# Optimization experiments

Measured on AMD Instinct MI355X. Metric: run time of the kernel, lower is better.

Reference implementation:

```python
import jax, jax.numpy as jnp
import numpy as np

H, KV, D = 12, 2, 128        # q heads, kv heads, head_dim
HID = 1536
B, S = 4, 2048               # equal-length packed sequences
T = B * S
EPS = 1e-6
ROPE_THETA = 10000.0


def _rms_norm(x, w):
    # RMSNorm over last dim in fp32, as in Qwen3RMSNorm
    xf = x.astype(jnp.float32)
    var = jnp.mean(xf * xf, axis=-1, keepdims=True)
    return (w * (xf * jax.lax.rsqrt(var + EPS))).astype(x.dtype)


def _apply_rope(x, cos, sin):
    # x: [T, h, D]; cos/sin: [T, D/2] -> expand over heads
    half = cos.shape[-1]
    x1, x2 = x[..., :half], x[..., half:2 * half]
    c = cos[:, None, :]
    s = sin[:, None, :]
    return jnp.concatenate([x1 * c - x2 * s, x1 * s + x2 * c], axis=-1)


def setup_inputs() -> dict:
    key = jax.random.key(0)
    ks = jax.random.split(key, 8)
    hidden_states = jax.random.normal(ks[0], (T, HID), dtype=jnp.float32)
    # real RoPE tables over per-sequence positions
    inv_freq = 1.0 / (ROPE_THETA ** (np.arange(0, D, 2, dtype=np.float32) / D))  # [D/2]
    pos = np.tile(np.arange(S, dtype=np.float32), B)                              # [T]
    ang = pos[:, None] * inv_freq[None, :]
    cos = jnp.asarray(np.cos(ang), dtype=jnp.float32)
    sin = jnp.asarray(np.sin(ang), dtype=jnp.float32)
    sc = 0.02
    Wq = jax.random.normal(ks[1], (HID, H * D), dtype=jnp.float32) * sc
    Wk = jax.random.normal(ks[2], (HID, KV * D), dtype=jnp.float32) * sc
    Wv = jax.random.normal(ks[3], (HID, KV * D), dtype=jnp.float32) * sc
    Wo = jax.random.normal(ks[4], (H * D, HID), dtype=jnp.float32) * sc
    q_norm_w = jnp.ones((D,), dtype=jnp.float32)
    k_norm_w = jnp.ones((D,), dtype=jnp.float32)
    cu_seqlens = jnp.arange(B + 1, dtype=jnp.int32) * S
    return {"hidden_states": hidden_states, "cos": cos, "sin": sin,
            "Wq": Wq, "Wk": Wk, "Wv": Wv, "Wo": Wo,
            "q_norm_w": q_norm_w, "k_norm_w": k_norm_w,
            "cu_seqlens": cu_seqlens}


def reference(hidden_states, cos, sin, Wq, Wk, Wv, Wo, q_norm_w, k_norm_w, cu_seqlens):
    # QKV projections on packed tokens
    q = (hidden_states @ Wq).reshape(T, H, D)
    k = (hidden_states @ Wk).reshape(T, KV, D)
    v = (hidden_states @ Wv).reshape(T, KV, D)
    # Qwen3 per-head QK RMSNorm, then RoPE
    q = _apply_rope(_rms_norm(q, q_norm_w), cos, sin)
    k = _apply_rope(_rms_norm(k, k_norm_w), cos, sin)
    # equal-length sequences: unpack to [B, h, S, D] (block-diagonal varlen attn)
    qb = q.reshape(B, S, H, D).transpose(0, 2, 1, 3)
    kb = k.reshape(B, S, KV, D).transpose(0, 2, 1, 3)
    vb = v.reshape(B, S, KV, D).transpose(0, 2, 1, 3)
    # GQA: repeat kv heads
    rep = H // KV
    kb = jnp.repeat(kb, rep, axis=1)
    vb = jnp.repeat(vb, rep, axis=1)
    scale = D ** -0.5
    scores = jnp.einsum('bhqd,bhkd->bhqk', qb, kb) * scale
    causal = jnp.tril(jnp.ones((S, S), dtype=bool))
    scores = jnp.where(causal[None, None], scores, jnp.finfo(scores.dtype).min)
    attn = jax.nn.softmax(scores, axis=-1)
    out = jnp.einsum('bhqk,bhkd->bhqd', attn, vb)       # [B,H,S,D]
    out = out.transpose(0, 2, 1, 3).reshape(T, H * D)   # repack
    return out @ Wo
```

## Files before the change

kernel.cpp:

```cpp
#include <hip/hip_runtime.h>
#include <hip/hip_bf16.h>
#include <stdint.h>

#define H_   12
#define KV_  2
#define D_   128
#define HID_ 1536
#define B_   4
#define S_   2048
#define T_   (B_*S_)

typedef __attribute__((ext_vector_type(8))) short  bf16x8;
typedef __attribute__((ext_vector_type(4))) float  f32x4;

__device__ __forceinline__ ushort f2bf(float f) {
  union { float f; uint32_t u; } v; v.f = f;
  uint32_t u = v.u;
  return (ushort)((u + 0x7fffu + ((u >> 16) & 1u)) >> 16);
}
__device__ __forceinline__ float bf2f(ushort u) {
  union { uint32_t u; float f; } v; v.u = ((uint32_t)u) << 16;
  return v.f;
}
__device__ __forceinline__ uint32_t cvtpk_bf16(float lo, float hi) {
  uint32_t r;
  asm("v_cvt_pk_bf16_f32 %0, %1, %2" : "=v"(r) : "v"(lo), "v"(hi));
  return r;
}

__device__ __forceinline__ void gload_lds16(const void* g, void* l) {
  __builtin_amdgcn_global_load_lds(
      (const __attribute__((address_space(1))) uint32_t*)g,
      (__attribute__((address_space(3))) uint32_t*)l, 16, 0, 0);
}

__global__ __launch_bounds__(256) void transpose_cvt2(const float* __restrict__ W0,
                                                      ushort* __restrict__ Wt0,
                                                      const float* __restrict__ W1,
                                                      ushort* __restrict__ Wt1,
                                                      int K, int N) {
  __shared__ float tile[32][33];
  const float* W  = blockIdx.z ? W1  : W0;
  ushort*      Wt = blockIdx.z ? Wt1 : Wt0;
  int k0 = blockIdx.x * 32, n0 = blockIdx.y * 32;
  int tx = threadIdx.x & 31, ty = threadIdx.x >> 5;
#pragma unroll
  for (int i = 0; i < 32; i += 8)
    tile[ty + i][tx] = W[(long)(k0 + ty + i) * N + n0 + tx];
  __syncthreads();
#pragma unroll
  for (int i = 0; i < 32; i += 8)
    Wt[(long)(n0 + ty + i) * K + k0 + tx] = f2bf(tile[tx][ty + i]);
}

template <int OUT_F32>
__global__ __launch_bounds__(256, 2) void gemm_bt(const ushort* __restrict__ A,
                                                  const ushort* __restrict__ Bt,
                                                  void* __restrict__ Cv,
                                                  int M, int N, int K, int lda) {
  __shared__ ushort lA[128 * 32];
  __shared__ ushort lB[128 * 32];
  const int tid = threadIdx.x;
  const int lane = tid & 63, w = tid >> 6;
  const int wr = w >> 1, wc = w & 1;
  const int l15 = lane & 15, lh = lane >> 4;
  const long m0 = (long)blockIdx.x * 128, n0 = (long)blockIdx.y * 128;
  const ushort* Ab = A + m0 * lda;
  const ushort* Bb = Bt + n0 * K;
  const int sr = tid >> 2;
  const int sc = (tid & 3) * 8;
  const int ldsoff = w * 512;
  f32x4 acc[4][4] = {};

  for (int k0 = 0; k0 < K; k0 += 32) {
#pragma unroll
    for (int it = 0; it < 2; ++it) {
      gload_lds16(Ab + (long)(it * 64 + sr) * lda + k0 + sc, &lA[it * 2048 + ldsoff]);
      gload_lds16(Bb + (long)(it * 64 + sr) * K + k0 + sc, &lB[it * 2048 + ldsoff]);
    }
    __syncthreads();
    bf16x8 af[4], bfr[4];
    const int ra = (wr * 64 + l15) * 32 + lh * 8;
    const int rb = (wc * 64 + l15) * 32 + lh * 8;
#pragma unroll
    for (int i = 0; i < 4; ++i) {
      af[i]  = *(const bf16x8*)&lA[ra + i * 16 * 32];
      bfr[i] = *(const bf16x8*)&lB[rb + i * 16 * 32];
    }
#pragma unroll
    for (int i = 0; i < 4; ++i)
#pragma unroll
      for (int j = 0; j < 4; ++j)
        acc[i][j] = __builtin_amdgcn_mfma_f32_16x16x32_bf16(af[i], bfr[j], acc[i][j], 0, 0, 0);
    __syncthreads();
  }
#pragma unroll
  for (int i = 0; i < 4; ++i) {
#pragma unroll
    for (int q = 0; q < 4; ++q) {
      long row = m0 + wr * 64 + i * 16 + lh * 4 + q;
#pragma unroll
      for (int j = 0; j < 4; ++j) {
        long col = n0 + wc * 64 + j * 16 + l15;
        float v = acc[i][j][q];
        if (OUT_F32) ((float*)Cv)[row * N + col] = v;
        else         ((ushort*)Cv)[row * N + col] = f2bf(v);
      }
    }
  }
}

__global__ __launch_bounds__(512) void gemm256f(const float* __restrict__ A32,
                                                const ushort* __restrict__ Bt,
                                                ushort* __restrict__ Cv,
                                                int M, int N, int K, int lda) {
  __shared__ ushort lA[2][256 * 64];
  __shared__ ushort lB[2][256 * 64];
  const int tid = threadIdx.x, lane = tid & 63;
  const int w = tid >> 6;
  const int l15 = lane & 15, lh = lane >> 4;
  const int wr = w >> 2, wc = w & 3;
  const long m0 = (long)blockIdx.x * 256, n0 = (long)blockIdx.y * 256;
  const float*  Ab = A32 + m0 * lda;
  const ushort* Bb = Bt + n0 * K;
  const int swz = (l15 & 7) << 4;

  f32x4 acc[8][4] = {};
  const int NT = K / 64;
  float4 areg[4][2];

#define ALOAD(KT) do {                                                        \
  const int k0s = (KT) * 64;                                                  \
  _Pragma("unroll") for (int it = 0; it < 4; ++it) {                          \
    int ch = it * 512 + tid; int r = ch >> 3, s = ch & 7;                     \
    const float* src = Ab + (long)r * lda + k0s + ((s ^ (r & 7)) * 8);        \
    areg[it][0] = *(const float4*)src;                                        \
    areg[it][1] = *(const float4*)(src + 4);                                  \
  }                                                                           \
} while (0)
#define AWRITE(PB) do {                                                       \
  _Pragma("unroll") for (int it = 0; it < 4; ++it) {                          \
    int ch = it * 512 + tid; int r = ch >> 3, s = ch & 7;                     \
    uint32_t pk0 = cvtpk_bf16(areg[it][0].x, areg[it][0].y);                  \
    uint32_t pk1 = cvtpk_bf16(areg[it][0].z, areg[it][0].w);                  \
    uint32_t pk2 = cvtpk_bf16(areg[it][1].x, areg[it][1].y);                  \
    uint32_t pk3 = cvtpk_bf16(areg[it][1].z, areg[it][1].w);                  \
    uint4 pk = make_uint4(pk0, pk1, pk2, pk3);                                \
    *(uint4*)&lA[PB][r * 64 + s * 8] = pk;                                    \
  }                                                                           \
} while (0)
#define BSTAGE(KT, PB) do {                                                   \
  const int k0s = (KT) * 64;                                                  \
  _Pragma("unroll") for (int it = 0; it < 4; ++it) {                          \
    int ch = it * 512 + tid; int r = ch >> 3, s = ch & 7;                     \
    int cb = it * 512 + (tid & 448);                                          \
    gload_lds16(Bb + (long)r * K + k0s + ((s ^ (r & 7)) * 8), &lB[PB][cb * 8]); \
  }                                                                           \
} while (0)

  ALOAD(0);
  BSTAGE(0, 0);
  AWRITE(0);
  __syncthreads();
  int p = 0;
  for (int kt = 0; kt < NT; ++kt) {
    if (kt + 1 < NT) { ALOAD(kt + 1); BSTAGE(kt + 1, p ^ 1); }
    const char* cA = (const char*)&lA[p][0];
    const char* cB = (const char*)&lB[p][0];
    bf16x8 bf[4][2];
#pragma unroll
    for (int fj = 0; fj < 4; ++fj)
#pragma unroll
      for (int kk = 0; kk < 2; ++kk)
        bf[fj][kk] = *(const bf16x8*)(cB + (wc * 64 + fj * 16 + l15) * 128 + ((kk * 64 + lh * 16) ^ swz));
    __builtin_amdgcn_s_setprio(1);
#pragma unroll
    for (int fi = 0; fi < 8; ++fi) {
      const int ra = (wr * 128 + fi * 16 + l15) * 128;
      bf16x8 af0 = *(const bf16x8*)(cA + ra + ((lh * 16) ^ swz));
      bf16x8 af1 = *(const bf16x8*)(cA + ra + ((64 + lh * 16) ^ swz));
#pragma unroll
      for (int fj = 0; fj < 4; ++fj) {
        acc[fi][fj] = __builtin_amdgcn_mfma_f32_16x16x32_bf16(af0, bf[fj][0], acc[fi][fj], 0, 0, 0);
        acc[fi][fj] = __builtin_amdgcn_mfma_f32_16x16x32_bf16(af1, bf[fj][1], acc[fi][fj], 0, 0, 0);
      }
    }
    __builtin_amdgcn_s_setprio(0);
    if (kt + 1 < NT) AWRITE(p ^ 1);
    __syncthreads();
    p ^= 1;
  }
#undef ALOAD
#undef AWRITE
#undef BSTAGE
#pragma unroll
  for (int fi = 0; fi < 8; ++fi) {
#pragma unroll
    for (int q = 0; q < 4; ++q) {
      long row = m0 + wr * 128 + fi * 16 + lh * 4 + q;
#pragma unroll
      for (int fj = 0; fj < 4; ++fj) {
        long col = n0 + wc * 64 + fj * 16 + l15;
        Cv[row * N + col] = f2bf(acc[fi][fj][q]);
      }
    }
  }
}

__global__ __launch_bounds__(256) void kv_prep(const ushort* __restrict__ QKV,
                                               const float* __restrict__ kw,
                                               const float* __restrict__ cosb,
                                               const float* __restrict__ sinb,
                                               ushort* __restrict__ Ka,
                                               ushort* __restrict__ Vt) {
  __shared__ ushort tile[32][33];
  const int tid = threadIdx.x, lane = tid & 63, w = tid >> 6;
  const int s0 = blockIdx.x * 32, bk = blockIdx.y;
  const int b = bk / KV_, g = bk % KV_;

#pragma unroll
  for (int j = 0; j < 8; ++j) {
    const int srow = s0 + w * 8 + j;
    const long t = (long)b * S_ + srow;
    const ushort* xr = QKV + t * 2048 + 1536 + g * 128;
    float x1 = bf2f(xr[lane]);
    float x2 = bf2f(xr[lane + 64]);
    float ss = x1 * x1 + x2 * x2;
#pragma unroll
    for (int off = 32; off; off >>= 1) ss += __shfl_xor(ss, off);
    float r = rsqrtf(ss * (1.0f / 128.0f) + 1e-6f);
    float y1 = x1 * r * kw[lane];
    float y2 = x2 * r * kw[lane + 64];
    float c = cosb[t * 64 + lane], s = sinb[t * 64 + lane];
    ushort* yr = Ka + ((long)bk * S_ + srow) * 128;
    yr[lane]      = f2bf(y1 * c - y2 * s);
    yr[lane + 64] = f2bf(y1 * s + y2 * c);
  }
  const int tx = tid & 31, ty = tid >> 5;
  for (int d0 = 0; d0 < 128; d0 += 32) {
    __syncthreads();
#pragma unroll
    for (int i = 0; i < 32; i += 8)
      tile[ty + i][tx] = QKV[(long)(b * S_ + s0 + ty + i) * 2048 + 1792 + g * 128 + d0 + tx];
    __syncthreads();
#pragma unroll
    for (int i = 0; i < 32; i += 8)
      Vt[(long)(bk * 128 + d0 + ty + i) * S_ + s0 + tx] = tile[tx][ty + i];
  }
}

__global__ __launch_bounds__(256, 2) void attn(ushort* __restrict__ QKV,
                                               const ushort* __restrict__ Ka,
                                               const ushort* __restrict__ Vt,
                                               const float* __restrict__ qnw,
                                               const float* __restrict__ cosb,
                                               const float* __restrict__ sinb) {
  __shared__ ushort lK[64 * 128];
  __shared__ ushort lV[128 * 64];
  __shared__ ushort lP[4 * 32 * 32];
  const int tid = threadIdx.x, lane = tid & 63, w = tid >> 6;
  const int l15 = lane & 15, lh = lane >> 4;
  char* cK = (char*)lK;
  char* cV = (char*)lV;
  char* cP = (char*)lP + w * 2048;
  const int swzK = l15 << 4;
  const int swzV = (l15 & 7) << 4;
  const int swzP = (l15 & 3) << 4;
  const float SCL = 0.08838834764831845f * 1.44269504088896f;
  const float M0  = 17.0f;

  const int qt = 15 - (int)(blockIdx.x / 48);
  const int bh = blockIdx.x % 48;
  const int b = bh / H_, h = bh % H_, g = h / (H_ / KV_);
  const int q0 = qt * 128;
  const ushort* Kb = Ka + (long)(b * KV_ + g) * S_ * 128;
  const ushort* Vb = Vt + (long)(b * KV_ + g) * 128 * S_;

  bf16x8 qf[2][4];
#pragma unroll
  for (int m = 0; m < 2; ++m) {
    const long tt = (long)b * S_ + q0 + w * 32 + m * 16 + l15;
    const ushort* xr = QKV + tt * 2048 + h * 128;
    bf16x8 raw[4];
#pragma unroll
    for (int kd = 0; kd < 4; ++kd)
      raw[kd] = *(const bf16x8*)&xr[kd * 32 + lh * 8];
    float ss = 0.f;
#pragma unroll
    for (int kd = 0; kd < 4; ++kd)
#pragma unroll
      for (int e = 0; e < 8; ++e) {
        float v = bf2f((ushort)raw[kd][e]);
        ss += v * v;
      }
    ss += __shfl_xor(ss, 16);
    ss += __shfl_xor(ss, 32);
    const float rn = rsqrtf(ss * (1.0f / 128.0f) + 1e-6f) * SCL;
    const float* cR = cosb + tt * 64;
    const float* sR = sinb + tt * 64;
#pragma unroll
    for (int kp = 0; kp < 2; ++kp) {
      bf16x8 qlo, qhi;
#pragma unroll
      for (int e = 0; e < 8; ++e) {
        const int ci = kp * 32 + lh * 8 + e;
        float c = cR[ci], s = sR[ci];
        float y1 = bf2f((ushort)raw[kp][e])     * rn * qnw[ci];
        float y2 = bf2f((ushort)raw[kp + 2][e]) * rn * qnw[64 + ci];
        qlo[e] = (short)f2bf(y1 * c - y2 * s);
        qhi[e] = (short)f2bf(y1 * s + y2 * c);
      }
      qf[m][kp]     = qlo;
      qf[m][kp + 2] = qhi;
    }
  }

  f32x4 o[2][8] = {};
  float lr[2] = {0.f, 0.f};
  const int nt = 2 * qt + 2;

  bf16x8 kreg[4], vreg[4];
#define LDTILE(K0) do { \
  _Pragma("unroll") for (int it = 0; it < 4; ++it) \
    kreg[it] = *(const bf16x8*)&Kb[(long)((K0) + it * 16 + (tid >> 4)) * 128 + (tid & 15) * 8]; \
  _Pragma("unroll") for (int it = 0; it < 4; ++it) \
    vreg[it] = *(const bf16x8*)&Vb[(long)(it * 32 + (tid >> 3)) * S_ + (K0) + (tid & 7) * 8]; \
} while (0)

  LDTILE(0);
  for (int t = 0; t < nt; ++t) {
    const int k0 = t * 64;
    __syncthreads();
#pragma unroll
    for (int it = 0; it < 4; ++it) {
      int r = it * 16 + (tid >> 4);
      *(bf16x8*)(cK + r * 256 + (((tid & 15) * 16) ^ (((tid >> 4) & 15) << 4))) = kreg[it];
    }
#pragma unroll
    for (int it = 0; it < 4; ++it) {
      int r = it * 32 + (tid >> 3);
      *(bf16x8*)(cV + r * 128 + (((tid & 7) * 16) ^ ((r & 7) << 4))) = vreg[it];
    }
    __syncthreads();
    if (t + 1 < nt) LDTILE(k0 + 64);

    if (k0 <= q0 + w * 32 + 31) {
      f32x4 sfr[2][4] = {};
      __builtin_amdgcn_s_setprio(1);
#pragma unroll
      for (int kd = 0; kd < 4; ++kd) {
        bf16x8 kf[4];
#pragma unroll
        for (int n = 0; n < 4; ++n)
          kf[n] = *(const bf16x8*)(cK + (n * 16 + l15) * 256 + ((kd * 64 + lh * 16) ^ swzK));
#pragma unroll
        for (int m = 0; m < 2; ++m)
#pragma unroll
          for (int n = 0; n < 4; ++n)
            sfr[m][n] = __builtin_amdgcn_mfma_f32_16x16x32_bf16(kf[n], qf[m][kd], sfr[m][n], 0, 0, 0);
      }
      __builtin_amdgcn_s_setprio(0);
      const bool boundary = (k0 + 63 > q0 + w * 32);
      if (boundary) {
#pragma unroll
        for (int m = 0; m < 2; ++m) {
          const int rowm = q0 + w * 32 + m * 16 + l15;
#pragma unroll
          for (int n = 0; n < 4; ++n) {
            int kb = k0 + n * 16 + lh * 4;
#pragma unroll
            for (int qr = 0; qr < 4; ++qr)
              if (kb + qr > rowm) sfr[m][n][qr] = -INFINITY;
          }
        }
      }
#pragma unroll
      for (int m = 0; m < 2; ++m) {
#pragma unroll
        for (int n = 0; n < 4; ++n) {
          float p0 = exp2f(sfr[m][n][0] - M0);
          float p1 = exp2f(sfr[m][n][1] - M0);
          float p2 = exp2f(sfr[m][n][2] - M0);
          float p3 = exp2f(sfr[m][n][3] - M0);
          sfr[m][n][0] = p0; sfr[m][n][1] = p1; sfr[m][n][2] = p2; sfr[m][n][3] = p3;
          lr[m] += (p0 + p1) + (p2 + p3);
        }
      }
#pragma unroll
      for (int kf2 = 0; kf2 < 2; ++kf2) {
#pragma unroll
        for (int m = 0; m < 2; ++m)
#pragma unroll
          for (int nl = 0; nl < 2; ++nl) {
            const int n = kf2 * 2 + nl;
            uint2 pk;
            pk.x = cvtpk_bf16(sfr[m][n][0], sfr[m][n][1]);
            pk.y = cvtpk_bf16(sfr[m][n][2], sfr[m][n][3]);
            *(uint2*)(cP + (m * 16 + l15) * 64 + ((nl * 32 + lh * 8) ^ swzP)) = pk;
          }
        const int cb = (lh * 16) ^ swzP;
        bf16x8 pf0 = *(const bf16x8*)(cP + l15 * 64 + cb);
        bf16x8 pf1 = *(const bf16x8*)(cP + (16 + l15) * 64 + cb);
        const int cv = (kf2 * 64 + lh * 16);
        __builtin_amdgcn_s_setprio(1);
#pragma unroll
        for (int dblk = 0; dblk < 8; ++dblk) {
          bf16x8 vf = *(const bf16x8*)(cV + (dblk * 16 + l15) * 128 + (cv ^ swzV));
          o[0][dblk] = __builtin_amdgcn_mfma_f32_16x16x32_bf16(pf0, vf, o[0][dblk], 0, 0, 0);
          o[1][dblk] = __builtin_amdgcn_mfma_f32_16x16x32_bf16(pf1, vf, o[1][dblk], 0, 0, 0);
        }
        __builtin_amdgcn_s_setprio(0);
      }
    }
  }
#undef LDTILE
#pragma unroll
  for (int m = 0; m < 2; ++m) {
    lr[m] += __shfl_xor(lr[m], 16);
    lr[m] += __shfl_xor(lr[m], 32);
    float inv = 1.f / lr[m];
#pragma unroll
    for (int qr = 0; qr < 4; ++qr) {
      float iv = __shfl(inv, lh * 4 + qr);
      long trow = (long)b * S_ + q0 + w * 32 + m * 16 + lh * 4 + qr;
#pragma unroll
      for (int dblk = 0; dblk < 8; ++dblk)
        QKV[trow * 2048 + h * 128 + dblk * 16 + l15] = f2bf(o[m][dblk][qr] * iv);
    }
  }
}

extern "C" void kernel_launch(void* const* d_in, const int* in_sizes, int n_in,
                              void* d_out, int out_size, void* d_ws, size_t ws_size,
                              hipStream_t stream) {
  const float* hs   = (const float*)d_in[0];
  const float* cosb = (const float*)d_in[1];
  const float* sinb = (const float*)d_in[2];
  const float* Wq   = (const float*)d_in[3];
  const float* Wk   = (const float*)d_in[4];
  const float* Wv   = (const float*)d_in[5];
  const float* Wo   = (const float*)d_in[6];
  const float* qw   = (const float*)d_in[7];
  const float* kw   = (const float*)d_in[8];
  (void)in_sizes; (void)n_in; (void)out_size; (void)ws_size;

  char* ws = (char*)d_ws;
  size_t off = 0;
  auto alloc = [&](size_t bytes) {
    void* p = ws + off;
    off += (bytes + 255) & ~(size_t)255;
    return p;
  };
  ushort* Wqt = (ushort*)alloc((size_t)HID_ * HID_ * 2);
  ushort* Wkt = (ushort*)alloc((size_t)256 * HID_ * 2);
  ushort* Wvt = (ushort*)alloc((size_t)256 * HID_ * 2);
  ushort* Wot = (ushort*)alloc((size_t)HID_ * HID_ * 2);
  ushort* qkv = (ushort*)alloc((size_t)T_ * 2048 * 2);
  ushort* ka  = (ushort*)alloc((size_t)T_ * 256 * 2);
  ushort* vt  = (ushort*)alloc((size_t)T_ * 256 * 2);

  transpose_cvt2<<<dim3(HID_ / 32, HID_ / 32, 2), 256, 0, stream>>>(Wq, Wqt, Wo, Wot, HID_, HID_);
  transpose_cvt2<<<dim3(HID_ / 32, 256 / 32, 2), 256, 0, stream>>>(Wk, Wkt, Wv, Wvt, HID_, 256);

  gemm256f<<<dim3(T_ / 256, 2048 / 256), 512, 0, stream>>>(hs, Wqt, qkv, T_, 2048, HID_, HID_);

  kv_prep<<<dim3(S_ / 32, B_ * KV_), 256, 0, stream>>>(qkv, kw, cosb, sinb, ka, vt);

  attn<<<768, 256, 0, stream>>>(qkv, ka, vt, qw, cosb, sinb);

  gemm_bt<1><<<dim3(T_ / 128, 1536 / 128), 256, 0, stream>>>(qkv, Wot, (float*)d_out, T_, 1536, HID_, 2048);
}
```

Before: 215.0 us.

## Double-buffer output GEMM with K=64 tiles and XOR-swizzled LDS

```diff
diff --git a/kernel.cpp b/kernel.cpp
--- a/kernel.cpp
+++ b/kernel.cpp
@@ -54,46 +54,67 @@
 }
 
 template <int OUT_F32>
-__global__ __launch_bounds__(256, 2) void gemm_bt(const ushort* __restrict__ A,
-                                                  const ushort* __restrict__ Bt,
-                                                  void* __restrict__ Cv,
-                                                  int M, int N, int K, int lda) {
-  __shared__ ushort lA[128 * 32];
-  __shared__ ushort lB[128 * 32];
-  const int tid = threadIdx.x;
-  const int lane = tid & 63, w = tid >> 6;
+__global__ __launch_bounds__(256) void gemm_bt64(const ushort* __restrict__ A,
+                                                 const ushort* __restrict__ Bt,
+                                                 void* __restrict__ Cv,
+                                                 int M, int N, int K, int lda) {
+  __shared__ ushort lA[2][128 * 64];
+  __shared__ ushort lB[2][128 * 64];
+  const int tid = threadIdx.x, lane = tid & 63, w = tid >> 6;
   const int wr = w >> 1, wc = w & 1;
   const int l15 = lane & 15, lh = lane >> 4;
   const long m0 = (long)blockIdx.x * 128, n0 = (long)blockIdx.y * 128;
   const ushort* Ab = A + m0 * lda;
   const ushort* Bb = Bt + n0 * K;
-  const int sr = tid >> 2;
-  const int sc = (tid & 3) * 8;
-  const int ldsoff = w * 512;
+  const int swz = (l15 & 7) << 4;
+
   f32x4 acc[4][4] = {};
-
-  for (int k0 = 0; k0 < K; k0 += 32) {
-#pragma unroll
-    for (int it = 0; it < 2; ++it) {
-      gload_lds16(Ab + (long)(it * 64 + sr) * lda + k0 + sc, &lA[it * 2048 + ldsoff]);
-      gload_lds16(Bb + (long)(it * 64 + sr) * K + k0 + sc, &lB[it * 2048 + ldsoff]);
-    }
-    __syncthreads();
-    bf16x8 af[4], bfr[4];
-    const int ra = (wr * 64 + l15) * 32 + lh * 8;
-    const int rb = (wc * 64 + l15) * 32 + lh * 8;
+  const int NT = K / 64;
+
+#define STG128(KT, PB) do {                                                        \
+  const int k0s = (KT) * 64;                                                       \
+  _Pragma("unroll") for (int it = 0; it < 4; ++it) {                               \
+    int ch = it * 256 + tid; int r = ch >> 3, s = ch & 7;                          \
+    int cb = it * 256 + (tid & 192);                                               \
+    gload_lds16(Ab + (long)r * lda + k0s + ((s ^ (r & 7)) * 8), &lA[PB][cb * 8]);  \
+  }                                                                                \
+  _Pragma("unroll") for (int it = 0; it < 4; ++it) {                               \
+    int ch = it * 256 + tid; int r = ch >> 3, s = ch & 7;                          \
+    int cb = it * 256 + (tid & 192);                                               \
+    gload_lds16(Bb + (long)r * K + k0s + ((s ^ (r & 7)) * 8), &lB[PB][cb * 8]);    \
+  }                                                                                \
+} while (0)
+
+  STG128(0, 0);
+  __syncthreads();
+  int p = 0;
+  for (int kt = 0; kt < NT; ++kt) {
+    if (kt + 1 < NT) STG128(kt + 1, p ^ 1);
+    const char* cA = (const char*)&lA[p][0];
+    const char* cB = (const char*)&lB[p][0];
+    bf16x8 bfr[4][2];
+#pragma unroll
+    for (int j = 0; j < 4; ++j)
+#pragma unroll
+      for (int kk = 0; kk < 2; ++kk)
+        bfr[j][kk] = *(const bf16x8*)(cB + (wc * 64 + j * 16 + l15) * 128 + ((kk * 64 + lh * 16) ^ swz));
+    __builtin_amdgcn_s_setprio(1);
 #pragma unroll
     for (int i = 0; i < 4; ++i) {
-      af[i]  = *(const bf16x8*)&lA[ra + i * 16 * 32];
-      bfr[i] = *(const bf16x8*)&lB[rb + i * 16 * 32];
-    }
-#pragma unroll
-    for (int i = 0; i < 4; ++i)
-#pragma unroll
-      for (int j = 0; j < 4; ++j)
-        acc[i][j] = __builtin_amdgcn_mfma_f32_16x16x32_bf16(af[i], bfr[j], acc[i][j], 0, 0, 0);
-    __syncthreads();
-  }
+      const int ra = (wr * 64 + i * 16 + l15) * 128;
+      bf16x8 af0 = *(const bf16x8*)(cA + ra + ((lh * 16) ^ swz));
+      bf16x8 af1 = *(const bf16x8*)(cA + ra + ((64 + lh * 16) ^ swz));
+#pragma unroll
+      for (int j = 0; j < 4; ++j) {
+        acc[i][j] = __builtin_amdgcn_mfma_f32_16x16x32_bf16(af0, bfr[j][0], acc[i][j], 0, 0, 0);
+        acc[i][j] = __builtin_amdgcn_mfma_f32_16x16x32_bf16(af1, bfr[j][1], acc[i][j], 0, 0, 0);
+      }
+    }
+    __builtin_amdgcn_s_setprio(0);
+    __syncthreads();
+    p ^= 1;
+  }
+#undef STG128
 #pragma unroll
   for (int i = 0; i < 4; ++i) {
 #pragma unroll
@@ -468,5 +489,5 @@
 
   attn<<<768, 256, 0, stream>>>(qkv, ka, vt, qw, cosb, sinb);
 
-  gemm_bt<1><<<dim3(T_ / 128, 1536 / 128), 256, 0, stream>>>(qkv, Wot, (float*)d_out, T_, 1536, HID_, 2048);
-}
+  gemm_bt64<1><<<dim3(T_ / 128, 1536 / 128), 256, 0, stream>>>(qkv, Wot, (float*)d_out, T_, 1536, HID_, 2048);
+}
```

New measurement: 222.4 us. 1.03x slower.
